# Performance work log

Measured on AMD Instinct MI355X. Metric: run time of the kernel, lower is better.

Reference implementation:

```python
import jax, jax.numpy as jnp
import numpy as np

T, B, C = 1024, 16, 1024
H, K, PAD_L = 16, 7, 3  # num_heads, kernel_size, padding_l
OUT = 1024


def setup_inputs() -> dict:
    key = jax.random.key(0)
    ks = jax.random.split(key, 8)
    s_in = 1.0 / np.sqrt(C)
    return {
        "x": jax.random.normal(ks[0], (T, B, C), dtype=jnp.float32),
        "W1": jax.random.normal(ks[1], (C, C), dtype=jnp.float32) * s_in,
        "b1": jnp.zeros((C,), dtype=jnp.float32),
        "Wq": jax.random.normal(ks[2], (C, H * K), dtype=jnp.float32) * s_in,
        "bq": jnp.zeros((H * K,), dtype=jnp.float32),
        "conv_bias": jax.random.normal(ks[3], (C,), dtype=jnp.float32) * 0.02,
        "W2": jax.random.normal(ks[4], (C, OUT), dtype=jnp.float32) * s_in,
        "b2": jnp.zeros((OUT,), dtype=jnp.float32),
    }


def reference(x, W1, b1, Wq, bq, conv_bias, W2, b2):
    # linear1 (glu=False -> no activation)
    h = x @ W1 + b1                       # [T, B, C]
    Tn, Bn, Cn = h.shape
    R = Cn // H                           # channels per head
    # dynamic filter prediction from query (= h), softmax over K taps
    w = (h @ Wq + bq).reshape(Tn, Bn, H, K)
    w = jax.nn.softmax(w, axis=-1)        # [T, B, H, K]
    # unfold1d: pad PAD_L left, K-1-PAD_L right along time, gather K-windows
    hp = jnp.pad(h, ((PAD_L, K - 1 - PAD_L), (0, 0), (0, 0)))
    win = jnp.stack([hp[k:k + Tn] for k in range(K)], axis=-1)  # [T, B, C, K]
    win = win.reshape(Tn, Bn, H, R, K)
    out = jnp.einsum('tbhrk,tbhk->tbhr', win, w).reshape(Tn, Bn, Cn)
    out = out + conv_bias                 # [T, B, C]
    return out @ W2 + b2                  # [T, B, OUT]
```

## Files before the change

### kernel.cpp

```cpp
#include <hip/hip_runtime.h>
#include <math.h>

#define T_DIM 1024
#define B_DIM 16
#define C_DIM 1024
#define H_DIM 16
#define K_TAPS 7
#define PAD_LEFT 3
#define OUT_DIM 1024
#define M_DIM (T_DIM * B_DIM)
#define HK 112
#define HKP 128
#define KD 1024

typedef __attribute__((ext_vector_type(8))) short bf16x8;
typedef __attribute__((ext_vector_type(4))) float f32x4;

__device__ __forceinline__ ushort f2bf(float f) {
    union { float f; unsigned u; } v; v.f = f;
    unsigned u = v.u;
    u += 0x7fffu + ((u >> 16) & 1u);
    return (ushort)(u >> 16);
}
__device__ __forceinline__ float bf2f(ushort h) {
    union { unsigned u; float f; } v; v.u = ((unsigned)h) << 16;
    return v.f;
}

__global__ __launch_bounds__(256) void prep(const float* __restrict__ x,
                                            ushort* __restrict__ xb,
                                            const float* __restrict__ W1s,
                                            const float* __restrict__ Wqs,
                                            const float* __restrict__ W2s,
                                            ushort* __restrict__ W1t,
                                            ushort* __restrict__ Wqt,
                                            ushort* __restrict__ W2t) {
    __shared__ float tile[32][33];
    const int bx = blockIdx.x;
    if (bx < 8192) {
        int i = bx * 256 + threadIdx.x;
        const float4* p = (const float4*)x;
        float4 a = p[2 * i], b = p[2 * i + 1];
        uint4 o;
        o.x = (unsigned)f2bf(a.x) | ((unsigned)f2bf(a.y) << 16);
        o.y = (unsigned)f2bf(a.z) | ((unsigned)f2bf(a.w) << 16);
        o.z = (unsigned)f2bf(b.x) | ((unsigned)f2bf(b.y) << 16);
        o.w = (unsigned)f2bf(b.z) | ((unsigned)f2bf(b.w) << 16);
        ((uint4*)xb)[i] = o;
        return;
    }
    int tb  = bx - 8192;
    int nbx = tb % 68;
    int k0  = (tb / 68) * 32;
    const float* W; ushort* Wt; int N, Npad, nb;
    if (nbx < 32)      { W = W1s; Wt = W1t; N = 1024; Npad = 1024; nb = nbx; }
    else if (nbx < 36) { W = Wqs; Wt = Wqt; N = 112;  Npad = 128;  nb = nbx - 32; }
    else               { W = W2s; Wt = W2t; N = 1024; Npad = 1024; nb = nbx - 36; }
    int n0 = nb * 32;
    int tx = threadIdx.x & 31, ty = threadIdx.x >> 5;
#pragma unroll
    for (int j = 0; j < 4; ++j) {
        int k = k0 + ty * 4 + j;
        int n = n0 + tx;
        tile[ty * 4 + j][tx] = (n < N) ? W[(size_t)k * N + n] : 0.f;
    }
    __syncthreads();
#pragma unroll
    for (int j = 0; j < 4; ++j) {
        int n = n0 + ty * 4 + j;
        if (n < Npad)
            Wt[(size_t)n * KD + k0 + tx] = f2bf(tile[tx][ty * 4 + j]);
    }
}

#define PHASE(P2KS, MH, READB, STAGE_STMT, VM_STMT)                           \
    {                                                                         \
        if (READB) {                                                          \
            _Pragma("unroll")                                                 \
            for (int n = 0; n < 4; ++n)                                       \
                b[n] = *(const bf16x8*)(Bbase + (P2KS)*8192 + bOff + n*512);  \
        }                                                                     \
        bf16x8 a_[4];                                                         \
        _Pragma("unroll")                                                     \
        for (int m = 0; m < 4; ++m)                                           \
            a_[m] = *(const bf16x8*)(Abase + (P2KS)*8192 + aOff +             \
                                     (MH)*2048 + m*512);                      \
        STAGE_STMT;                                                           \
        VM_STMT;                                                              \
        __builtin_amdgcn_s_barrier();                                         \
        asm volatile("s_waitcnt lgkmcnt(0)" ::: "memory");                    \
        __builtin_amdgcn_sched_barrier(0);                                    \
        __builtin_amdgcn_s_setprio(1);                                        \
        _Pragma("unroll")                                                     \
        for (int m = 0; m < 4; ++m)                                           \
            _Pragma("unroll")                                                 \
            for (int n = 0; n < 4; ++n)                                       \
                acc[(MH)*4 + m][n] = __builtin_amdgcn_mfma_f32_16x16x32_bf16( \
                    a_[m], b[n], acc[(MH)*4 + m][n], 0, 0, 0);                \
        __builtin_amdgcn_s_setprio(0);                                        \
        __builtin_amdgcn_s_barrier();                                         \
        __builtin_amdgcn_sched_barrier(0);                                    \
    }

template <bool OUT_BF16>
__global__ __launch_bounds__(512, 1) void gemm8p(
    const ushort* __restrict__ A, const ushort* __restrict__ Bt,
    const float* __restrict__ bias, void* __restrict__ Cp, int ldc) {
    __shared__ ushort Lds[8 * 8192];

    const int tid  = threadIdx.x;
    const int lane = tid & 63;
    const int wid  = tid >> 6;
    const int wr = wid >> 2;
    const int wc = wid & 3;
    const int fr = lane & 15;
    const int fq = lane >> 4;

    const int orig = blockIdx.x;
    const int nid  = (orig & 7) * 32 + (orig >> 3);
    const int bm = (nid >> 2) * 256;
    const int bn = (nid & 3) * 256;

    const int srow = tid >> 2;
    const int scol = ((tid & 3) ^ ((tid >> 3) & 3)) * 8;
    const size_t sA = (size_t)(bm + srow) * KD + scol;
    const size_t sB = (size_t)(bn + srow) * KD + scol;
    const int sdst = wid * 64 * 8;

    const int slotSw = (fq ^ ((fr >> 1) & 3)) * 8;
    const int aOff = (wr * 128 + fr) * 32 + slotSw;
    const int bOff = (wc * 64 + fr) * 32 + slotSw;
    const ushort* Abase = &Lds[0];
    const ushort* Bbase = &Lds[4 * 8192];

    f32x4 acc[8][4];
#pragma unroll
    for (int m = 0; m < 8; ++m)
#pragma unroll
        for (int n = 0; n < 4; ++n) acc[m][n] = (f32x4){0.f, 0.f, 0.f, 0.f};

    auto stageA = [&](int slot, int koff) {
#pragma unroll
        for (int i = 0; i < 2; ++i)
            __builtin_amdgcn_global_load_lds(
                (const __attribute__((address_space(1))) void*)(A + sA + koff + (size_t)i * 128 * KD),
                (__attribute__((address_space(3))) void*)(&Lds[slot * 8192 + i * 4096 + sdst]),
                16, 0, 0);
    };
    auto stageB = [&](int slot, int koff) {
#pragma unroll
        for (int i = 0; i < 2; ++i)
            __builtin_amdgcn_global_load_lds(
                (const __attribute__((address_space(1))) void*)(Bt + sB + koff + (size_t)i * 128 * KD),
                (__attribute__((address_space(3))) void*)(&Lds[(4 + slot) * 8192 + i * 4096 + sdst]),
                16, 0, 0);
    };

    stageA(0, 0);   stageB(0, 0);
    stageA(1, 32);  stageB(1, 32);
    stageA(2, 64);  stageB(2, 64);
    stageA(3, 96);  stageB(3, 96);
    asm volatile("s_waitcnt vmcnt(12)" ::: "memory");
    __builtin_amdgcn_sched_barrier(0);
    __builtin_amdgcn_s_barrier();
    __builtin_amdgcn_sched_barrier(0);

#pragma unroll 1
    for (int j = 0; j < 8; ++j) {
        bf16x8 b[4];
        const int e = 2 * j;

        PHASE(0, 0, 1,
              { if (j >= 1) stageA(3, (e + 1) * 64 + 32); },
              { asm volatile("s_waitcnt vmcnt(6)" ::: "memory");
                __builtin_amdgcn_sched_barrier(0); })
        PHASE(0, 1, 0,
              { if (j >= 1) stageB(3, (e + 1) * 64 + 32); },
              (void)0; )
        PHASE(1, 0, 1,
              { if (j < 7) stageA(0, (e + 2) * 64); },
              { if (j == 7) { asm volatile("s_waitcnt vmcnt(4)" ::: "memory");
                              __builtin_amdgcn_sched_barrier(0); } })
        PHASE(1, 1, 0,
              { if (j < 7) stageB(0, (e + 2) * 64); },
              (void)0; )
        PHASE(2, 0, 1,
              { if (j < 7) stageA(1, (e + 2) * 64 + 32); },
              { if (j == 7) { asm volatile("s_waitcnt vmcnt(0)" ::: "memory"); }
                else        { asm volatile("s_waitcnt vmcnt(6)" ::: "memory"); }
                __builtin_amdgcn_sched_barrier(0); })
        PHASE(2, 1, 0,
              { if (j < 7) stageB(1, (e + 2) * 64 + 32); },
              (void)0; )
        PHASE(3, 0, 1,
              { if (j < 7) stageA(2, (e + 3) * 64); },
              (void)0; )
        PHASE(3, 1, 0,
              { if (j < 7) stageB(2, (e + 3) * 64); },
              (void)0; )
    }

#pragma unroll
    for (int n = 0; n < 4; ++n) {
        int col = bn + wc * 64 + n * 16 + fr;
        float bv = bias[col];
#pragma unroll
        for (int m = 0; m < 8; ++m) {
#pragma unroll
            for (int r = 0; r < 4; ++r) {
                int row = bm + wr * 128 + m * 16 + fq * 4 + r;
                float v = acc[m][n][r] + bv;
                if (OUT_BF16)
                    ((ushort*)Cp)[(size_t)row * ldc + col] = f2bf(v);
                else
                    ((float*)Cp)[(size_t)row * ldc + col] = v;
            }
        }
    }
}

__global__ __launch_bounds__(256) void gemm_small(const ushort* __restrict__ A,
                                                  const ushort* __restrict__ Bt,
                                                  const float* __restrict__ bias,
                                                  float* __restrict__ Cp) {
    __shared__ ushort Als[64 * 32];
    __shared__ ushort Bls[128 * 32];
    const int tid  = threadIdx.x;
    const int lane = tid & 63;
    const int wid  = tid >> 6;
    const int wr = wid >> 1, wc = wid & 1;
    const int bm = blockIdx.y * 64;
    const int fq = lane >> 4, fr = lane & 15;

    f32x4 acc[2][4];
#pragma unroll
    for (int m = 0; m < 2; ++m)
#pragma unroll
        for (int n = 0; n < 4; ++n) acc[m][n] = (f32x4){0.f, 0.f, 0.f, 0.f};

    const int rA = tid >> 2, oA = (tid & 3) * 8;
    for (int k0 = 0; k0 < KD; k0 += 32) {
        __builtin_amdgcn_global_load_lds(
            (const __attribute__((address_space(1))) void*)&A[(size_t)(bm + rA) * KD + k0 + oA],
            (__attribute__((address_space(3))) void*)&Als[wid * 64 * 8], 16, 0, 0);
#pragma unroll
        for (int i = 0; i < 2; ++i) {
            int c = i * 256 + tid;
            __builtin_amdgcn_global_load_lds(
                (const __attribute__((address_space(1))) void*)&Bt[(size_t)(c >> 2) * KD + k0 + (c & 3) * 8],
                (__attribute__((address_space(3))) void*)&Bls[(i * 256 + wid * 64) * 8], 16, 0, 0);
        }
        __syncthreads();

        bf16x8 af[2], bfr[4];
#pragma unroll
        for (int m = 0; m < 2; ++m)
            af[m] = *(const bf16x8*)&Als[(wr * 32 + m * 16 + fr) * 32 + fq * 8];
#pragma unroll
        for (int n = 0; n < 4; ++n)
            bfr[n] = *(const bf16x8*)&Bls[(wc * 64 + n * 16 + fr) * 32 + fq * 8];
#pragma unroll
        for (int m = 0; m < 2; ++m)
#pragma unroll
            for (int n = 0; n < 4; ++n)
                acc[m][n] = __builtin_amdgcn_mfma_f32_16x16x32_bf16(
                    af[m], bfr[n], acc[m][n], 0, 0, 0);
        __syncthreads();
    }

#pragma unroll
    for (int m = 0; m < 2; ++m) {
#pragma unroll
        for (int n = 0; n < 4; ++n) {
            int col = wc * 64 + n * 16 + fr;
            if (col >= HK) continue;
            float bv = bias[col];
#pragma unroll
            for (int r = 0; r < 4; ++r) {
                int row = bm + wr * 32 + m * 16 + fq * 4 + r;
                Cp[(size_t)row * HK + col] = acc[m][n][r] + bv;
            }
        }
    }
}

__global__ __launch_bounds__(256) void dynconv2(const ushort* __restrict__ h,
                                                const float* __restrict__ q,
                                                const float* __restrict__ cbias,
                                                ushort* __restrict__ out) {
    __shared__ ushort hw[22][1024];
    __shared__ float wsm[16][HK];
    const int tid = threadIdx.x;
    const int b  = blockIdx.x & 15;
    const int t0 = (blockIdx.x >> 4) << 4;

    for (int i = tid; i < 22 * 128; i += 256) {
        int wrow = i >> 7;
        int c8   = (i & 127) * 8;
        int tt   = t0 + wrow - PAD_LEFT;
        uint4 v = make_uint4(0, 0, 0, 0);
        if (tt >= 0 && tt < T_DIM)
            v = *(const uint4*)&h[((size_t)tt * B_DIM + b) * C_DIM + c8];
        *(uint4*)&hw[wrow][c8] = v;
    }
    {
        int tl = tid >> 4, hh = tid & 15;
        int m = (t0 + tl) * B_DIM + b;
        const float* p = &q[(size_t)m * HK + hh * K_TAPS];
        float mx = p[0];
#pragma unroll
        for (int k = 1; k < K_TAPS; ++k) mx = fmaxf(mx, p[k]);
        float e[K_TAPS], s = 0.f;
#pragma unroll
        for (int k = 0; k < K_TAPS; ++k) { e[k] = __expf(p[k] - mx); s += e[k]; }
        float inv = 1.f / s;
#pragma unroll
        for (int k = 0; k < K_TAPS; ++k) wsm[tl][hh * K_TAPS + k] = e[k] * inv;
    }
    __syncthreads();

    const int c  = tid * 4;
    const int hh = c >> 6;
    float4 bias = *(const float4*)&cbias[c];

    for (int tl = 0; tl < 16; ++tl) {
        float a0 = bias.x, a1 = bias.y, a2 = bias.z, a3 = bias.w;
#pragma unroll
        for (int k = 0; k < K_TAPS; ++k) {
            ushort4 hv = *(const ushort4*)&hw[tl + k][c];
            float wk = wsm[tl][hh * K_TAPS + k];
            a0 = fmaf(bf2f(hv.x), wk, a0);
            a1 = fmaf(bf2f(hv.y), wk, a1);
            a2 = fmaf(bf2f(hv.z), wk, a2);
            a3 = fmaf(bf2f(hv.w), wk, a3);
        }
        ushort4 o;
        o.x = f2bf(a0); o.y = f2bf(a1); o.z = f2bf(a2); o.w = f2bf(a3);
        *(ushort4*)&out[((size_t)(t0 + tl) * B_DIM + b) * C_DIM + c] = o;
    }
}

extern "C" void kernel_launch(void* const* d_in, const int* in_sizes, int n_in,
                              void* d_out, int out_size, void* d_ws,
                              size_t ws_size, hipStream_t stream) {
    const float* x     = (const float*)d_in[0];
    const float* W1    = (const float*)d_in[1];
    const float* b1    = (const float*)d_in[2];
    const float* Wq    = (const float*)d_in[3];
    const float* bq    = (const float*)d_in[4];
    const float* cbias = (const float*)d_in[5];
    const float* W2    = (const float*)d_in[6];
    const float* b2    = (const float*)d_in[7];
    float* out = (float*)d_out;

    ushort* xb    = (ushort*)d_ws;
    ushort* hb    = xb    + (size_t)M_DIM * C_DIM;
    ushort* convb = hb    + (size_t)M_DIM * C_DIM;
    ushort* W1t   = convb + (size_t)M_DIM * C_DIM;
    ushort* W2t   = W1t   + (size_t)C_DIM * C_DIM;
    ushort* Wqt   = W2t   + (size_t)C_DIM * OUT_DIM;
    float*  q     = (float*)(Wqt + (size_t)HKP * C_DIM);

    prep<<<dim3(8192 + 68 * 32), dim3(256), 0, stream>>>(
        x, xb, W1, Wq, W2, W1t, Wqt, W2t);

    gemm8p<true><<<dim3(256), dim3(512), 0, stream>>>(xb, W1t, b1, hb, C_DIM);

    gemm_small<<<dim3(1, M_DIM / 64), dim3(256), 0, stream>>>(hb, Wqt, bq, q);

    dynconv2<<<dim3(B_DIM * T_DIM / 16), dim3(256), 0, stream>>>(
        hb, q, cbias, convb);

    gemm8p<false><<<dim3(256), dim3(512), 0, stream>>>(convb, W2t, b2, out,
                                                       OUT_DIM);
}
```

Before: 148.1 us.

## Merge half-tile GEMM phases into one phase per K-slot

Restructures the main GEMM loop so each K-slot runs as a single phase that loads all 8 A fragments and 4 B fragments, then issues 32 MFMAs, instead of two half phases of 16 MFMAs each. The A and B staging for the next slot is issued together, and the vmcnt waits are retuned to match. This halves the number of block barriers per iteration and lengthens each uninterrupted MFMA run. In exchange it raises register pressure from holding 8 A fragments at once and gives less fine-grained overlap between loads and compute.

```diff
diff --git a/kernel.cpp b/kernel.cpp
--- a/kernel.cpp
+++ b/kernel.cpp
@@ -73,18 +73,16 @@
     }
 }
 
-#define PHASE(P2KS, MH, READB, STAGE_STMT, VM_STMT)                           \
+#define MPHASE(SLOT, STAGE_STMT, VM_STMT)                                     \
     {                                                                         \
-        if (READB) {                                                          \
-            _Pragma("unroll")                                                 \
-            for (int n = 0; n < 4; ++n)                                       \
-                b[n] = *(const bf16x8*)(Bbase + (P2KS)*8192 + bOff + n*512);  \
-        }                                                                     \
-        bf16x8 a_[4];                                                         \
+        bf16x8 b[4], a_[8];                                                   \
         _Pragma("unroll")                                                     \
-        for (int m = 0; m < 4; ++m)                                           \
-            a_[m] = *(const bf16x8*)(Abase + (P2KS)*8192 + aOff +             \
-                                     (MH)*2048 + m*512);                      \
+        for (int n = 0; n < 4; ++n)                                           \
+            b[n] = *(const bf16x8*)(Bbase + (SLOT)*8192 + bOff + n*512);      \
+        _Pragma("unroll")                                                     \
+        for (int m = 0; m < 8; ++m)                                           \
+            a_[m] = *(const bf16x8*)(Abase + (SLOT)*8192 + aOff +             \
+                                     (m >> 2)*2048 + (m & 3)*512);            \
         STAGE_STMT;                                                           \
         VM_STMT;                                                              \
         __builtin_amdgcn_s_barrier();                                         \
@@ -92,11 +90,11 @@
         __builtin_amdgcn_sched_barrier(0);                                    \
         __builtin_amdgcn_s_setprio(1);                                        \
         _Pragma("unroll")                                                     \
-        for (int m = 0; m < 4; ++m)                                           \
+        for (int m = 0; m < 8; ++m)                                           \
             _Pragma("unroll")                                                 \
             for (int n = 0; n < 4; ++n)                                       \
-                acc[(MH)*4 + m][n] = __builtin_amdgcn_mfma_f32_16x16x32_bf16( \
-                    a_[m], b[n], acc[(MH)*4 + m][n], 0, 0, 0);                \
+                acc[m][n] = __builtin_amdgcn_mfma_f32_16x16x32_bf16(          \
+                    a_[m], b[n], acc[m][n], 0, 0, 0);                         \
         __builtin_amdgcn_s_setprio(0);                                        \
         __builtin_amdgcn_s_barrier();                                         \
         __builtin_amdgcn_sched_barrier(0);                                    \
@@ -167,37 +165,30 @@
 
 #pragma unroll 1
     for (int j = 0; j < 8; ++j) {
-        bf16x8 b[4];
         const int e = 2 * j;
 
-        PHASE(0, 0, 1,
-              { if (j >= 1) stageA(3, (e + 1) * 64 + 32); },
-              { asm volatile("s_waitcnt vmcnt(6)" ::: "memory");
-                __builtin_amdgcn_sched_barrier(0); })
-        PHASE(0, 1, 0,
-              { if (j >= 1) stageB(3, (e + 1) * 64 + 32); },
-              (void)0; )
-        PHASE(1, 0, 1,
-              { if (j < 7) stageA(0, (e + 2) * 64); },
-              { if (j == 7) { asm volatile("s_waitcnt vmcnt(4)" ::: "memory");
+        MPHASE(0,
+               { if (j >= 1) { stageA(3, (e + 1) * 64 + 32);
+                               stageB(3, (e + 1) * 64 + 32); } },
+               { asm volatile("s_waitcnt vmcnt(8)" ::: "memory");
+                 __builtin_amdgcn_sched_barrier(0); })
+        MPHASE(1,
+               { if (j < 7) { stageA(0, (e + 2) * 64);
+                              stageB(0, (e + 2) * 64); } },
+               { if (j == 7) { asm volatile("s_waitcnt vmcnt(4)" ::: "memory"); }
+                 else        { asm volatile("s_waitcnt vmcnt(8)" ::: "memory"); }
+                 __builtin_amdgcn_sched_barrier(0); })
+        MPHASE(2,
+               { if (j < 7) { stageA(1, (e + 2) * 64 + 32);
+                              stageB(1, (e + 2) * 64 + 32); } },
+               { if (j == 7) { asm volatile("s_waitcnt vmcnt(0)" ::: "memory"); }
+                 else        { asm volatile("s_waitcnt vmcnt(8)" ::: "memory"); }
+                 __builtin_amdgcn_sched_barrier(0); })
+        MPHASE(3,
+               { if (j < 7) { stageA(2, (e + 3) * 64);
+                              stageB(2, (e + 3) * 64); } },
+               { if (j < 7) { asm volatile("s_waitcnt vmcnt(8)" ::: "memory");
                               __builtin_amdgcn_sched_barrier(0); } })
-        PHASE(1, 1, 0,
-              { if (j < 7) stageB(0, (e + 2) * 64); },
-              (void)0; )
-        PHASE(2, 0, 1,
-              { if (j < 7) stageA(1, (e + 2) * 64 + 32); },
-              { if (j == 7) { asm volatile("s_waitcnt vmcnt(0)" ::: "memory"); }
-                else        { asm volatile("s_waitcnt vmcnt(6)" ::: "memory"); }
-                __builtin_amdgcn_sched_barrier(0); })
-        PHASE(2, 1, 0,
-              { if (j < 7) stageB(1, (e + 2) * 64 + 32); },
-              (void)0; )
-        PHASE(3, 0, 1,
-              { if (j < 7) stageA(2, (e + 3) * 64); },
-              (void)0; )
-        PHASE(3, 1, 0,
-              { if (j < 7) stageB(2, (e + 3) * 64); },
-              (void)0; )
     }
 
 #pragma unroll
```

After: 147.3 us. No clear change (-0.6%).
